# Kernel tuning notes

Hardware: AMD Instinct MI355X
Metric: run time of the kernel (lower is better)

Reference implementation:

```python
import jax, jax.numpy as jnp
import numpy as np

K = 5          # k = min(5, min(S, T)) with S = T = 4096
SIGMA = 1.0
EPS_VAR = 1e-08
EPS_LOG = 1e-08


def _entropy(p):
    # sum(-p * log2(clamp(p, 1e-8)), axis=1).mean()
    return jnp.sum(-p * jnp.log2(jnp.clip(p, EPS_LOG, None)), axis=1).mean()


def _pairwise_dist(x):
    # Euclidean cdist via GEMM (matches torch's use_mm_for_euclid path)
    sq = jnp.sum(x * x, axis=1)                       # [N]
    d2 = sq[:, None] + sq[None, :] - 2.0 * (x @ x.T)  # [N, N]
    d2 = jnp.maximum(d2, 0.0)
    # safe sqrt (zero diagonal) — value identical, grad-safe
    return jnp.where(d2 > 0, jnp.sqrt(jnp.where(d2 > 0, d2, 1.0)), 0.0)


def _row_var(block):
    # sqrt(k-th smallest distance per row + eps): max of k smallest
    kth = -jax.lax.top_k(-block, K)[0][:, -1]
    return jnp.sqrt(kth + EPS_VAR)                    # [rows]


def _sim(block, var_row, zero_diag):
    s = jnp.exp(-block / (2.0 * (var_row[:, None] * SIGMA) ** 2))
    if zero_diag:
        n = block.shape[0]
        s = s * (1.0 - jnp.eye(n, dtype=s.dtype))
    return s


def _forward(Feature_all, logit_all, y_source):
    S = y_source.shape[0]
    logit_source = logit_all[:S]
    logit_target = logit_all[S:]

    # cross-entropy on source
    logp = jax.nn.log_softmax(logit_source, axis=1)
    loss_cl = -jnp.take_along_axis(logp, y_source[:, None], axis=1).mean()

    # entropy of target softmax
    loss_ce = _entropy(jax.nn.softmax(logit_target, axis=1))

    # reg_loss_dist
    dist = _pairwise_dist(Feature_all)                # [N, N]
    d_ss = dist[:S, :S]
    d_st = dist[:S, S:]
    d_tt = dist[S:, S:]
    d_ts = dist[S:, :S]

    sim_ss = _sim(d_ss, _row_var(d_ss), True)
    sim_st = _sim(d_st, _row_var(d_st), False)
    sim_tt = _sim(d_tt, _row_var(d_tt), True)
    sim_ts = _sim(d_ts, _row_var(d_ts), False)

    src_intra = jnp.max(sim_ss, axis=1)
    src_inter = jnp.max(sim_st, axis=1)
    tgt_intra = jnp.max(sim_tt, axis=1)
    tgt_inter = jnp.max(sim_ts, axis=1)

    loss_reg = (jnp.abs(src_intra - src_inter).mean()
                + jnp.abs(tgt_intra - tgt_inter).mean())
    return loss_cl, loss_ce, loss_reg


def setup_inputs() -> dict:
    key = jax.random.key(0)
    k1, k2, k3 = jax.random.split(key, 3)
    N, D, C, S = 8192, 256, 65, 4096
    return {
        "Feature_all": jax.random.normal(k1, (N, D), dtype=jnp.float32),
        "logit_all": jax.random.normal(k2, (N, C), dtype=jnp.float32),
        "y_source": jax.random.randint(k3, (S,), 0, C, dtype=jnp.int64
                                       if jax.config.jax_enable_x64 else jnp.int32),
        "device": 0,
    }


def reference(Feature_all, logit_all, y_source, device):
    del device  # torch-specific, ignored
    return _forward(Feature_all, logit_all, y_source)
```

## Files before the change

### kernel.cpp

```cpp
#include <hip/hip_runtime.h>
#include <stdint.h>

#define Nn 8192
#define Dd 256
#define Ss 4096
#define Cc 65

#define TI 128
#define TJ 128
#define BK 32
#define CHUNK 512
#define NCHUNK (Nn / CHUNK)
#define NJT (CHUNK / TJ)
#define KS (Dd / BK)

#define BIGF 3.0e37f

typedef float f4 __attribute__((ext_vector_type(4)));
typedef __bf16 bf8 __attribute__((ext_vector_type(8)));

__device__ __forceinline__ float wredsum(float v) {
#pragma unroll
  for (int o = 32; o; o >>= 1) v += __shfl_xor(v, o, 64);
  return v;
}
__device__ __forceinline__ float wredmax(float v) {
#pragma unroll
  for (int o = 32; o; o >>= 1) v = fmaxf(v, __shfl_xor(v, o, 64));
  return v;
}

__device__ __forceinline__ unsigned short f2bf(float f) {
  unsigned int u = __float_as_uint(f);
  u = (u + 0x7fffu + ((u >> 16) & 1u)) >> 16;
  return (unsigned short)u;
}

__device__ __forceinline__ void merge5(const float* a, const float* b, float* o) {
  o[0] = fminf(a[0], b[0]);
  o[1] = fminf(fminf(a[1], b[1]), fmaxf(a[0], b[0]));
  o[2] = fminf(fminf(a[2], b[2]), fminf(fmaxf(a[1], b[0]), fmaxf(a[0], b[1])));
  o[3] = fminf(fminf(a[3], b[3]), fminf(fmaxf(a[2], b[0]), fminf(fmaxf(a[1], b[1]), fmaxf(a[0], b[2]))));
  o[4] = fminf(fminf(a[4], b[4]),
               fminf(fmaxf(a[3], b[0]),
                     fminf(fmaxf(a[2], b[1]), fminf(fmaxf(a[1], b[2]), fmaxf(a[0], b[3])))));
}

__global__ __launch_bounds__(256) void prep_loss_kernel(const float* __restrict__ X,
                                                        unsigned short* __restrict__ xb,
                                                        float* __restrict__ sqn,
                                                        const float* __restrict__ logit,
                                                        const int* __restrict__ y,
                                                        float* __restrict__ part_cl,
                                                        float* __restrict__ part_ce,
                                                        unsigned int* __restrict__ counter) {
  if (blockIdx.x == 0 && threadIdx.x == 0) *counter = 0u;
  int lane = threadIdx.x & 63;
  if (blockIdx.x < 2048) {
    int row = blockIdx.x * 4 + (threadIdx.x >> 6);
    f4 v = ((const f4*)(X + (size_t)row * Dd))[lane];
    float ss = v[0] * v[0] + v[1] * v[1] + v[2] * v[2] + v[3] * v[3];
    ss = wredsum(ss);
    if (lane == 0) sqn[row] = ss;
    ushort4 o;
    o.x = f2bf(v[0]); o.y = f2bf(v[1]); o.z = f2bf(v[2]); o.w = f2bf(v[3]);
    ((ushort4*)(xb + (size_t)row * Dd))[lane] = o;
  } else {
    int bid = blockIdx.x - 2048;
    int row = bid * 4 + (threadIdx.x >> 6);
    const float* xr = logit + (size_t)row * Cc;
    float x1 = xr[lane];
    float x2 = (lane == 0) ? xr[64] : -BIGF;
    float mx = wredmax(fmaxf(x1, x2));
    float e1 = expf(x1 - mx);
    float e2 = (lane == 0) ? expf(x2 - mx) : 0.f;
    float Z = wredsum(e1 + e2);
    float res;
    if (row < Ss) {
      int yy = y[row];
      float pick = (lane == yy ? x1 : 0.f) + ((lane == 0 && yy == 64) ? x2 : 0.f);
      float xy = wredsum(pick);
      res = -(xy - mx - logf(Z));
    } else {
      float p1 = e1 / Z;
      float t1 = -p1 * log2f(fmaxf(p1, 1e-8f));
      if (lane == 0) {
        float p2 = e2 / Z;
        t1 += -p2 * log2f(fmaxf(p2, 1e-8f));
      }
      res = wredsum(t1);
    }
    __shared__ float a4[4];
    if (lane == 0) a4[threadIdx.x >> 6] = res;
    __syncthreads();
    if (threadIdx.x == 0) {
      float s = a4[0] + a4[1] + a4[2] + a4[3];
      if (bid < 1024) part_cl[bid] = s;
      else part_ce[bid - 1024] = s;
    }
  }
}

__device__ __forceinline__ void stage16(const void* g, void* l) {
  __builtin_amdgcn_global_load_lds((__attribute__((address_space(1))) void*)g,
                                   (__attribute__((address_space(3))) void*)l, 16, 0, 0);
}

__global__ __launch_bounds__(256) void dist_kernel(const unsigned short* __restrict__ xb,
                                                   const float* __restrict__ sqn,
                                                   float* __restrict__ top5ws) {
  __shared__ unsigned short ldsA[2][TJ * BK];
  __shared__ unsigned short ldsB[2][TI * BK];

  const int tid = threadIdx.x;
  const int lane = tid & 63;
  const int wv = tid >> 6;
  const int q = lane >> 4;
  const int c = lane & 15;
  const int jw = wv & 1;
  const int iw = wv >> 1;

  const int ib = (blockIdx.x / NCHUNK) * TI;
  const int chunk = blockIdx.x % NCHUNK;
  const int jc0 = chunk * CHUNK;

  const int swz = q ^ ((lane >> 1) & 3);
  const int pr = lane >> 2;
  const int qd = (lane & 3) ^ ((lane >> 3) & 3);
  const int u0 = wv * 2, u1 = wv * 2 + 1;
  const int gcol = qd * 8;

  float top[4][5];
#pragma unroll
  for (int a = 0; a < 4; ++a)
#pragma unroll
    for (int b = 0; b < 5; ++b) top[a][b] = BIGF;

  const int iwbase = ib + iw * 64;

  for (int jt = 0; jt < NJT; ++jt) {
    const int jb = jc0 + jt * TJ;

    f4 acc[4][4];
    f4 z = {0.f, 0.f, 0.f, 0.f};
#pragma unroll
    for (int a = 0; a < 4; ++a)
#pragma unroll
      for (int b2 = 0; b2 < 4; ++b2) acc[a][b2] = z;

    stage16(xb + (size_t)(jb + u0 * 16 + pr) * Dd + gcol, &ldsA[0][u0 * 512]);
    stage16(xb + (size_t)(jb + u1 * 16 + pr) * Dd + gcol, &ldsA[0][u1 * 512]);
    stage16(xb + (size_t)(ib + u0 * 16 + pr) * Dd + gcol, &ldsB[0][u0 * 512]);
    stage16(xb + (size_t)(ib + u1 * 16 + pr) * Dd + gcol, &ldsB[0][u1 * 512]);
    __syncthreads();

#pragma unroll
    for (int ks = 0; ks < KS; ++ks) {
      const int b = ks & 1;
      if (ks + 1 < KS) {
        const int k0 = (ks + 1) * BK;
        stage16(xb + (size_t)(jb + u0 * 16 + pr) * Dd + k0 + gcol, &ldsA[b ^ 1][u0 * 512]);
        stage16(xb + (size_t)(jb + u1 * 16 + pr) * Dd + k0 + gcol, &ldsA[b ^ 1][u1 * 512]);
        stage16(xb + (size_t)(ib + u0 * 16 + pr) * Dd + k0 + gcol, &ldsB[b ^ 1][u0 * 512]);
        stage16(xb + (size_t)(ib + u1 * 16 + pr) * Dd + k0 + gcol, &ldsB[b ^ 1][u1 * 512]);
      }
      bf8 aF[4], bF[4];
#pragma unroll
      for (int rt = 0; rt < 4; ++rt)
        aF[rt] = *(const bf8*)&ldsA[b][(jw * 64 + rt * 16 + c) * 32 + swz * 8];
#pragma unroll
      for (int ct = 0; ct < 4; ++ct)
        bF[ct] = *(const bf8*)&ldsB[b][(iw * 64 + ct * 16 + c) * 32 + swz * 8];
#pragma unroll
      for (int rt = 0; rt < 4; ++rt)
#pragma unroll
        for (int ct = 0; ct < 4; ++ct)
          acc[rt][ct] = __builtin_amdgcn_mfma_f32_16x16x32_bf16(aF[rt], bF[ct], acc[rt][ct], 0, 0, 0);
      __syncthreads();
    }

    const int jrow = jb + jw * 64;
    f4 sq4[4];
#pragma unroll
    for (int rt = 0; rt < 4; ++rt) sq4[rt] = *(const f4*)&sqn[jrow + rt * 16 + q * 4];
    const bool mayDiag = (jrow == iwbase);
#pragma unroll
    for (int ct = 0; ct < 4; ++ct) {
      float t[16];
#pragma unroll
      for (int rt = 0; rt < 4; ++rt)
#pragma unroll
        for (int r = 0; r < 4; ++r)
          t[rt * 4 + r] = fmaf(acc[rt][ct][r], -2.0f, sq4[rt][r]);
      if (mayDiag && ((c >> 2) == q)) t[ct * 4 + (c & 3)] = BIGF;
      float tm = fminf(fminf(fminf(fminf(t[0], t[1]), fminf(t[2], t[3])),
                             fminf(fminf(t[4], t[5]), fminf(t[6], t[7]))),
                       fminf(fminf(fminf(t[8], t[9]), fminf(t[10], t[11])),
                             fminf(fminf(t[12], t[13]), fminf(t[14], t[15]))));
      if (tm < top[ct][4]) {
#pragma unroll
        for (int kk = 0; kk < 16; ++kk) {
          float x = t[kk];
          if (x < top[ct][4]) {
#pragma unroll
            for (int s = 0; s < 4; ++s) {
              float lo = fminf(top[ct][s], x);
              x = fmaxf(top[ct][s], x);
              top[ct][s] = lo;
            }
            top[ct][4] = x;
          }
        }
      }
    }
  }

  float fin[4][5];
#pragma unroll
  for (int ct = 0; ct < 4; ++ct) {
    float a0 = top[ct][0], a1 = top[ct][1], a2 = top[ct][2], a3 = top[ct][3], a4 = top[ct][4];
#pragma unroll
    for (int off = 16; off <= 32; off <<= 1) {
      float b0 = __shfl_xor(a0, off, 64);
      float b1 = __shfl_xor(a1, off, 64);
      float b2 = __shfl_xor(a2, off, 64);
      float b3 = __shfl_xor(a3, off, 64);
      float b4 = __shfl_xor(a4, off, 64);
      float c0 = fminf(a0, b0);
      float c1 = fminf(fminf(a1, b1), fmaxf(a0, b0));
      float c2 = fminf(fminf(a2, b2), fminf(fmaxf(a1, b0), fmaxf(a0, b1)));
      float c3 = fminf(fminf(a3, b3), fminf(fmaxf(a2, b0), fminf(fmaxf(a1, b1), fmaxf(a0, b2))));
      float c4 = fminf(fminf(a4, b4),
                       fminf(fmaxf(a3, b0),
                             fminf(fmaxf(a2, b1), fminf(fmaxf(a1, b2), fmaxf(a0, b3)))));
      a0 = c0; a1 = c1; a2 = c2; a3 = c3; a4 = c4;
    }
    fin[ct][0] = a0; fin[ct][1] = a1; fin[ct][2] = a2; fin[ct][3] = a3; fin[ct][4] = a4;
  }

  float* mbuf = (float*)ldsA;
  if (jw == 1 && q == 0) {
#pragma unroll
    for (int ct = 0; ct < 4; ++ct) {
      float* m = mbuf + ((((iw << 2) | ct) << 4) + c) * 5;
      m[0] = fin[ct][0]; m[1] = fin[ct][1]; m[2] = fin[ct][2]; m[3] = fin[ct][3]; m[4] = fin[ct][4];
    }
  }
  __syncthreads();
  if (jw == 0 && q == 0) {
#pragma unroll
    for (int ct = 0; ct < 4; ++ct) {
      const float* m = mbuf + ((((iw << 2) | ct) << 4) + c) * 5;
      float bl[5] = {m[0], m[1], m[2], m[3], m[4]};
      float o[5];
      merge5(fin[ct], bl, o);
      int i = iwbase + ct * 16 + c;
      float* dst = top5ws + ((size_t)i * NCHUNK + chunk) * 5;
      dst[0] = o[0]; dst[1] = o[1]; dst[2] = o[2]; dst[3] = o[3]; dst[4] = o[4];
    }
  }
}

__device__ __forceinline__ void merge8lists(const float* L, float* o) {
  float m01[5], m23[5], m45[5], m67[5], mA[5], mB[5];
  merge5(L + 0, L + 5, m01);
  merge5(L + 10, L + 15, m23);
  merge5(L + 20, L + 25, m45);
  merge5(L + 30, L + 35, m67);
  merge5(m01, m23, mA);
  merge5(m45, m67, mB);
  merge5(mA, mB, o);
}

__global__ __launch_bounds__(256) void reg_final_kernel(const float* __restrict__ top5ws,
                                                        const float* __restrict__ sqn,
                                                        float* __restrict__ part_reg,
                                                        const float* __restrict__ part_cl,
                                                        const float* __restrict__ part_ce,
                                                        float* __restrict__ out,
                                                        unsigned int* __restrict__ counter) {
  int i = blockIdx.x * 256 + threadIdx.x;
  float buf[80];
  const float* L = top5ws + (size_t)i * 80;
#pragma unroll
  for (int k = 0; k < 80; ++k) buf[k] = L[k];
  float mlo[5], mhi[5];
  merge8lists(buf, mlo);
  merge8lists(buf + 40, mhi);
  bool srcRow = (i < Ss);
  float A0 = srcRow ? mlo[0] : mhi[0];
  float A3 = srcRow ? mlo[3] : mhi[3];
  float B0 = srcRow ? mhi[0] : mlo[0];
  float B4 = srcRow ? mhi[4] : mlo[4];
  float sq = sqn[i];
  float dmin_a = sqrtf(fmaxf(A0 + sq, 0.f));
  float kth_a = sqrtf(fmaxf(A3 + sq, 0.f));
  float dmin_b = sqrtf(fmaxf(B0 + sq, 0.f));
  float kth_b = sqrtf(fmaxf(B4 + sq, 0.f));
  float sa = expf(-dmin_a / (2.f * (kth_a + 1e-8f)));
  float sb = expf(-dmin_b / (2.f * (kth_b + 1e-8f)));
  float v = fabsf(sa - sb);
  __shared__ float red[256];
  red[threadIdx.x] = v;
  __syncthreads();
#pragma unroll
  for (int s = 128; s; s >>= 1) {
    if (threadIdx.x < s) red[threadIdx.x] += red[threadIdx.x + s];
    __syncthreads();
  }
  if (threadIdx.x == 0) part_reg[blockIdx.x] = red[0];

  __shared__ unsigned int lastFlag;
  __threadfence();
  if (threadIdx.x == 0) lastFlag = (atomicAdd(counter, 1u) == 31u) ? 1u : 0u;
  __syncthreads();
  if (!lastFlag) return;
  __threadfence();

  __shared__ double dred[256];
  int tid = threadIdx.x;
  double a = 0.0;
  for (int k = tid; k < 1024; k += 256) a += (double)part_cl[k];
  dred[tid] = a; __syncthreads();
  for (int s = 128; s; s >>= 1) { if (tid < s) dred[tid] += dred[tid + s]; __syncthreads(); }
  double cl = dred[0]; __syncthreads();
  a = 0.0;
  for (int k = tid; k < 1024; k += 256) a += (double)part_ce[k];
  dred[tid] = a; __syncthreads();
  for (int s = 128; s; s >>= 1) { if (tid < s) dred[tid] += dred[tid + s]; __syncthreads(); }
  double ce = dred[0]; __syncthreads();
  a = (tid < 16) ? (double)part_reg[tid] : 0.0;
  dred[tid] = a; __syncthreads();
  for (int s = 128; s; s >>= 1) { if (tid < s) dred[tid] += dred[tid + s]; __syncthreads(); }
  double rs = dred[0]; __syncthreads();
  a = (tid >= 16 && tid < 32) ? (double)part_reg[tid] : 0.0;
  dred[tid] = a; __syncthreads();
  for (int s = 128; s; s >>= 1) { if (tid < s) dred[tid] += dred[tid + s]; __syncthreads(); }
  if (tid == 0) {
    out[0] = (float)(cl / 4096.0);
    out[1] = (float)(ce / 4096.0);
    out[2] = (float)(rs / 4096.0 + dred[0] / 4096.0);
  }
}

extern "C" void kernel_launch(void* const* d_in, const int* in_sizes, int n_in,
                              void* d_out, int out_size, void* d_ws, size_t ws_size,
                              hipStream_t stream) {
  (void)in_sizes; (void)n_in; (void)out_size; (void)ws_size;
  const float* X = (const float*)d_in[0];
  const float* logit = (const float*)d_in[1];
  const int* y = (const int*)d_in[2];
  float* out = (float*)d_out;
  char* ws = (char*)d_ws;

  unsigned short* xb = (unsigned short*)ws;
  float* sqn = (float*)(ws + (4u << 20));
  float* top5 = (float*)(ws + (4u << 20) + (64u << 10));
  float* part_cl = (float*)(ws + (7u << 20));
  float* part_ce = part_cl + 1024;
  float* part_reg = part_ce + 1024;
  unsigned int* counter = (unsigned int*)(part_reg + 32);

  hipLaunchKernelGGL(prep_loss_kernel, dim3(4096), dim3(256), 0, stream, X, xb, sqn, logit, y,
                     part_cl, part_ce, counter);
  hipLaunchKernelGGL(dist_kernel, dim3((Nn / TI) * NCHUNK), dim3(256), 0, stream, xb, sqn, top5);
  hipLaunchKernelGGL(reg_final_kernel, dim3(32), dim3(256), 0, stream, top5, sqn, part_reg,
                     part_cl, part_ce, out, counter);
}
```

Before: 156.5 us.

## Keep full-K B tile resident in LDS and widen chunks with 8-wave blocks

The distance kernel now loads the whole 128-row i-tile across all of K into LDS once per block and reuses it for every j-tile in the chunk. Only the j-tile stays double-buffered. Chunks double to 1024 columns and blocks grow to 512 threads, so each wave covers 64x32 instead of 64x64. This cuts redundant global-to-LDS traffic for the i operand and halves the per-row partial top-5 lists the final kernel merges. In exchange it needs more LDS per block (about 80KB) and launches half as many blocks, which may reduce latency hiding and occupancy.

```diff
diff --git a/kernel.cpp b/kernel.cpp
--- a/kernel.cpp
+++ b/kernel.cpp
@@ -9,7 +9,7 @@
 #define TI 128
 #define TJ 128
 #define BK 32
-#define CHUNK 512
+#define CHUNK 1024
 #define NCHUNK (Nn / CHUNK)
 #define NJT (CHUNK / TJ)
 #define KS (Dd / BK)
@@ -106,11 +106,11 @@
                                    (__attribute__((address_space(3))) void*)l, 16, 0, 0);
 }
 
-__global__ __launch_bounds__(256) void dist_kernel(const unsigned short* __restrict__ xb,
-                                                   const float* __restrict__ sqn,
-                                                   float* __restrict__ top5ws) {
+__global__ __launch_bounds__(512, 4) void dist_kernel(const unsigned short* __restrict__ xb,
+                                                      const float* __restrict__ sqn,
+                                                      float* __restrict__ top5ws) {
   __shared__ unsigned short ldsA[2][TJ * BK];
-  __shared__ unsigned short ldsB[2][TI * BK];
+  __shared__ unsigned short ldsBf[KS][TI * BK];
 
   const int tid = threadIdx.x;
   const int lane = tid & 63;
@@ -118,7 +118,7 @@
   const int q = lane >> 4;
   const int c = lane & 15;
   const int jw = wv & 1;
-  const int iw = wv >> 1;
+  const int iq = wv >> 1;
 
   const int ib = (blockIdx.x / NCHUNK) * TI;
   const int chunk = blockIdx.x % NCHUNK;
@@ -127,54 +127,50 @@
   const int swz = q ^ ((lane >> 1) & 3);
   const int pr = lane >> 2;
   const int qd = (lane & 3) ^ ((lane >> 3) & 3);
-  const int u0 = wv * 2, u1 = wv * 2 + 1;
   const int gcol = qd * 8;
 
-  float top[4][5];
-#pragma unroll
-  for (int a = 0; a < 4; ++a)
+  float top[2][5];
+#pragma unroll
+  for (int a = 0; a < 2; ++a)
 #pragma unroll
     for (int b = 0; b < 5; ++b) top[a][b] = BIGF;
 
-  const int iwbase = ib + iw * 64;
+  const int iwbase = ib + iq * 32;
+
+#pragma unroll
+  for (int ks = 0; ks < KS; ++ks)
+    stage16(xb + (size_t)(ib + wv * 16 + pr) * Dd + ks * BK + gcol, &ldsBf[ks][wv * 512]);
 
   for (int jt = 0; jt < NJT; ++jt) {
     const int jb = jc0 + jt * TJ;
 
-    f4 acc[4][4];
+    f4 acc[4][2];
     f4 z = {0.f, 0.f, 0.f, 0.f};
 #pragma unroll
     for (int a = 0; a < 4; ++a)
 #pragma unroll
-      for (int b2 = 0; b2 < 4; ++b2) acc[a][b2] = z;
-
-    stage16(xb + (size_t)(jb + u0 * 16 + pr) * Dd + gcol, &ldsA[0][u0 * 512]);
-    stage16(xb + (size_t)(jb + u1 * 16 + pr) * Dd + gcol, &ldsA[0][u1 * 512]);
-    stage16(xb + (size_t)(ib + u0 * 16 + pr) * Dd + gcol, &ldsB[0][u0 * 512]);
-    stage16(xb + (size_t)(ib + u1 * 16 + pr) * Dd + gcol, &ldsB[0][u1 * 512]);
+      for (int b2 = 0; b2 < 2; ++b2) acc[a][b2] = z;
+
+    stage16(xb + (size_t)(jb + wv * 16 + pr) * Dd + gcol, &ldsA[0][wv * 512]);
     __syncthreads();
 
 #pragma unroll
     for (int ks = 0; ks < KS; ++ks) {
       const int b = ks & 1;
-      if (ks + 1 < KS) {
-        const int k0 = (ks + 1) * BK;
-        stage16(xb + (size_t)(jb + u0 * 16 + pr) * Dd + k0 + gcol, &ldsA[b ^ 1][u0 * 512]);
-        stage16(xb + (size_t)(jb + u1 * 16 + pr) * Dd + k0 + gcol, &ldsA[b ^ 1][u1 * 512]);
-        stage16(xb + (size_t)(ib + u0 * 16 + pr) * Dd + k0 + gcol, &ldsB[b ^ 1][u0 * 512]);
-        stage16(xb + (size_t)(ib + u1 * 16 + pr) * Dd + k0 + gcol, &ldsB[b ^ 1][u1 * 512]);
-      }
-      bf8 aF[4], bF[4];
+      if (ks + 1 < KS)
+        stage16(xb + (size_t)(jb + wv * 16 + pr) * Dd + (ks + 1) * BK + gcol,
+                &ldsA[b ^ 1][wv * 512]);
+      bf8 aF[4], bF[2];
 #pragma unroll
       for (int rt = 0; rt < 4; ++rt)
         aF[rt] = *(const bf8*)&ldsA[b][(jw * 64 + rt * 16 + c) * 32 + swz * 8];
 #pragma unroll
-      for (int ct = 0; ct < 4; ++ct)
-        bF[ct] = *(const bf8*)&ldsB[b][(iw * 64 + ct * 16 + c) * 32 + swz * 8];
+      for (int ct = 0; ct < 2; ++ct)
+        bF[ct] = *(const bf8*)&ldsBf[ks][(iq * 32 + ct * 16 + c) * 32 + swz * 8];
 #pragma unroll
       for (int rt = 0; rt < 4; ++rt)
 #pragma unroll
-        for (int ct = 0; ct < 4; ++ct)
+        for (int ct = 0; ct < 2; ++ct)
           acc[rt][ct] = __builtin_amdgcn_mfma_f32_16x16x32_bf16(aF[rt], bF[ct], acc[rt][ct], 0, 0, 0);
       __syncthreads();
     }
@@ -183,16 +179,17 @@
     f4 sq4[4];
 #pragma unroll
     for (int rt = 0; rt < 4; ++rt) sq4[rt] = *(const f4*)&sqn[jrow + rt * 16 + q * 4];
-    const bool mayDiag = (jrow == iwbase);
-#pragma unroll
-    for (int ct = 0; ct < 4; ++ct) {
+    const bool mayDiag = (jb == ib) && ((iq >> 1) == jw);
+#pragma unroll
+    for (int ct = 0; ct < 2; ++ct) {
       float t[16];
 #pragma unroll
       for (int rt = 0; rt < 4; ++rt)
 #pragma unroll
         for (int r = 0; r < 4; ++r)
           t[rt * 4 + r] = fmaf(acc[rt][ct][r], -2.0f, sq4[rt][r]);
-      if (mayDiag && ((c >> 2) == q)) t[ct * 4 + (c & 3)] = BIGF;
+      if (mayDiag && ((c >> 2) == q))
+        t[((iq & 1) * 2 + ct) * 4 + (c & 3)] = BIGF;
       float tm = fminf(fminf(fminf(fminf(t[0], t[1]), fminf(t[2], t[3])),
                              fminf(fminf(t[4], t[5]), fminf(t[6], t[7]))),
                        fminf(fminf(fminf(t[8], t[9]), fminf(t[10], t[11])),
@@ -215,9 +212,9 @@
     }
   }
 
-  float fin[4][5];
-#pragma unroll
-  for (int ct = 0; ct < 4; ++ct) {
+  float fin[2][5];
+#pragma unroll
+  for (int ct = 0; ct < 2; ++ct) {
     float a0 = top[ct][0], a1 = top[ct][1], a2 = top[ct][2], a3 = top[ct][3], a4 = top[ct][4];
 #pragma unroll
     for (int off = 16; off <= 32; off <<= 1) {
@@ -241,16 +238,16 @@
   float* mbuf = (float*)ldsA;
   if (jw == 1 && q == 0) {
 #pragma unroll
-    for (int ct = 0; ct < 4; ++ct) {
-      float* m = mbuf + ((((iw << 2) | ct) << 4) + c) * 5;
+    for (int ct = 0; ct < 2; ++ct) {
+      float* m = mbuf + ((((iq << 1) | ct) << 4) + c) * 5;
       m[0] = fin[ct][0]; m[1] = fin[ct][1]; m[2] = fin[ct][2]; m[3] = fin[ct][3]; m[4] = fin[ct][4];
     }
   }
   __syncthreads();
   if (jw == 0 && q == 0) {
 #pragma unroll
-    for (int ct = 0; ct < 4; ++ct) {
-      const float* m = mbuf + ((((iw << 2) | ct) << 4) + c) * 5;
+    for (int ct = 0; ct < 2; ++ct) {
+      const float* m = mbuf + ((((iq << 1) | ct) << 4) + c) * 5;
       float bl[5] = {m[0], m[1], m[2], m[3], m[4]};
       float o[5];
       merge5(fin[ct], bl, o);
@@ -261,15 +258,11 @@
   }
 }
 
-__device__ __forceinline__ void merge8lists(const float* L, float* o) {
-  float m01[5], m23[5], m45[5], m67[5], mA[5], mB[5];
+__device__ __forceinline__ void merge4lists(const float* L, float* o) {
+  float m01[5], m23[5];
   merge5(L + 0, L + 5, m01);
   merge5(L + 10, L + 15, m23);
-  merge5(L + 20, L + 25, m45);
-  merge5(L + 30, L + 35, m67);
-  merge5(m01, m23, mA);
-  merge5(m45, m67, mB);
-  merge5(mA, mB, o);
+  merge5(m01, m23, o);
 }
 
 __global__ __launch_bounds__(256) void reg_final_kernel(const float* __restrict__ top5ws,
@@ -280,13 +273,13 @@
                                                         float* __restrict__ out,
                                                         unsigned int* __restrict__ counter) {
   int i = blockIdx.x * 256 + threadIdx.x;
-  float buf[80];
-  const float* L = top5ws + (size_t)i * 80;
-#pragma unroll
-  for (int k = 0; k < 80; ++k) buf[k] = L[k];
+  float buf[40];
+  const float* L = top5ws + (size_t)i * 40;
+#pragma unroll
+  for (int k = 0; k < 40; ++k) buf[k] = L[k];
   float mlo[5], mhi[5];
-  merge8lists(buf, mlo);
-  merge8lists(buf + 40, mhi);
+  merge4lists(buf, mlo);
+  merge4lists(buf + 20, mhi);
   bool srcRow = (i < Ss);
   float A0 = srcRow ? mlo[0] : mhi[0];
   float A3 = srcRow ? mlo[3] : mhi[3];
@@ -363,7 +356,7 @@
 
   hipLaunchKernelGGL(prep_loss_kernel, dim3(4096), dim3(256), 0, stream, X, xb, sqn, logit, y,
                      part_cl, part_ce, counter);
-  hipLaunchKernelGGL(dist_kernel, dim3((Nn / TI) * NCHUNK), dim3(256), 0, stream, xb, sqn, top5);
+  hipLaunchKernelGGL(dist_kernel, dim3((Nn / TI) * NCHUNK), dim3(512), 0, stream, xb, sqn, top5);
   hipLaunchKernelGGL(reg_final_kernel, dim3(32), dim3(256), 0, stream, top5, sqn, part_reg,
                      part_cl, part_ce, out, counter);
 }
```

Result: faster. 141.4 us (-9.6%).
